# Kernel optimization log

Measured on AMD Instinct MI355X. Metric: run time of the kernel, lower is better.

The kernel has to match this reference:

```python
import jax, jax.numpy as jnp
import numpy as np


def setup_inputs() -> dict:
    key = jax.random.key(0)
    ks = jax.random.split(key, 5)
    B, S, I, H, O = 64, 2048, 128, 512, 128
    inputs = jax.random.normal(ks[0], (B, S, I), dtype=jnp.float32)
    h0 = jnp.zeros((B, H), dtype=jnp.float32)
    # Xavier-uniform for W_in / W_out, orthogonal-ish scaled for W_rec
    lim_in = float(np.sqrt(6.0 / (I + H)))
    W_in_w = jax.random.uniform(ks[1], (H, I), minval=-lim_in, maxval=lim_in, dtype=jnp.float32)
    W_in_b = jnp.zeros((H,), dtype=jnp.float32)
    # orthogonal init scaled by 0.9 (matches nn.init.orthogonal_ * 0.9)
    A = jax.random.normal(ks[2], (H, H), dtype=jnp.float32)
    Q, _ = jnp.linalg.qr(A)
    W_rec_w = (0.9 * Q).astype(jnp.float32)
    lim_out = float(np.sqrt(6.0 / (H + O)))
    W_out_w = jax.random.uniform(ks[3], (O, H), minval=-lim_out, maxval=lim_out, dtype=jnp.float32)
    W_out_b = jnp.zeros((O,), dtype=jnp.float32)
    return {
        "inputs": inputs, "h0": h0,
        "W_in_w": W_in_w, "W_in_b": W_in_b,
        "W_rec_w": W_rec_w,
        "W_out_w": W_out_w, "W_out_b": W_out_b,
    }


def reference(inputs, h0, W_in_w, W_in_b, W_rec_w, W_out_w, W_out_b):
    # Precompute the input projection for all timesteps in one big GEMM:
    # (B, S, I) @ (I, H) -> (B, S, H). Faithful: W_in(x_t) = x_t @ W_in_w.T + b.
    xin = jnp.einsum('bsi,hi->bsh', inputs, W_in_w) + W_in_b

    def step(h, x_t):  # x_t: (B, H) pre-projected input at time t
        h_new = jnp.tanh(x_t + h @ W_rec_w.T)  # W_rec has no bias
        return h_new, h_new

    # scan over time axis; move time to leading axis
    h_final, hs = jax.lax.scan(step, h0, jnp.swapaxes(xin, 0, 1))  # hs: (S, B, H)
    hs = jnp.swapaxes(hs, 0, 1)  # (B, S, H)
    outputs = jnp.einsum('bsh,oh->bso', hs, W_out_w) + W_out_b  # (B, S, O)
    return outputs, h_final
```

## Files before the change

kernel.cpp:

```cpp
#include <hip/hip_runtime.h>


typedef _Float16 half2_t __attribute__((ext_vector_type(2)));
typedef _Float16 half8_t __attribute__((ext_vector_type(8)));
typedef float    float2_t __attribute__((ext_vector_type(2)));
typedef float    float4_t __attribute__((ext_vector_type(4)));

#define BB 64
#define SS 2048
#define IN 128
#define HH 512
#define OO 128

using u32 = unsigned int;
using u64 = unsigned long long;

__device__ __forceinline__ float fdot2f(half2_t a, half2_t b, float c) {
#if __has_builtin(__builtin_amdgcn_fdot2)
    return __builtin_amdgcn_fdot2(a, b, c, false);
#else
    return c + (float)a[0] * (float)b[0] + (float)a[1] * (float)b[1];
#endif
}
__device__ __forceinline__ half2_t h2(float a, float b) {
    return half2_t{(_Float16)a, (_Float16)b};
}

__device__ __forceinline__ float fast_tanh(float x) {
    x = fminf(8.0f, fmaxf(-8.0f, x));
#if __has_builtin(__builtin_amdgcn_exp2f) && __has_builtin(__builtin_amdgcn_rcpf)
    const float t = __builtin_amdgcn_exp2f(x * 2.885390081777927f);
    return 1.0f - 2.0f * __builtin_amdgcn_rcpf(t + 1.0f);
#else
    return tanhf(x);
#endif
}

__device__ __forceinline__ void barrier_lds() {
    asm volatile("s_waitcnt lgkmcnt(0)\n\ts_barrier" ::: "memory");
}

__global__ __launch_bounds__(512, 1) void rnn_fused(
    const float* __restrict__ inputs,
    const float* __restrict__ h0,
    const float* __restrict__ W_in,
    const float* __restrict__ W_in_b,
    const float* __restrict__ W_rec,
    const float* __restrict__ W_out,
    const float* __restrict__ W_out_b,
    float* __restrict__ outp,
    float* __restrict__ hfinal,
    u64* __restrict__ hex)
{
    const int tid = threadIdx.x;
    const int bb = blockIdx.x >> 1;
    const int w  = blockIdx.x & 1;
    const int c  = tid & 7;
    const int q  = tid >> 3;
    const int og = w * 64 + q;
    const int s  = c >> 2;
    const int oc = w * 4 + (c & 3);
    const int pc = (1 - w) * 4 + (c & 3);
    const int pw = 1 - w;

    __shared__ __align__(16) half2_t hbuf[288];
    __shared__ __align__(16) half2_t xh[2][96];

    half2_t wro[4][16];
    half2_t wrp[4][16];
    half2_t wi[4][8];
    half2_t woo[16];
    half2_t wop[16];
    float bias[4];

    #pragma unroll
    for (int jj = 0; jj < 4; ++jj) {
        const int jg = w * 256 + q * 4 + jj;
        const float4_t* ro = (const float4_t*)(W_rec + jg * HH + oc * 64 + s * 32);
        const float4_t* rp = (const float4_t*)(W_rec + jg * HH + pc * 64 + s * 32);
        #pragma unroll
        for (int m = 0; m < 8; ++m) {
            const float4_t uo = ro[m];
            wro[jj][m * 2 + 0] = h2(uo[0], uo[1]);
            wro[jj][m * 2 + 1] = h2(uo[2], uo[3]);
            const float4_t up = rp[m];
            wrp[jj][m * 2 + 0] = h2(up[0], up[1]);
            wrp[jj][m * 2 + 1] = h2(up[2], up[3]);
        }
        const float4_t* irow = (const float4_t*)(W_in + jg * IN + c * 16);
        #pragma unroll
        for (int m = 0; m < 4; ++m) {
            const float4_t u = irow[m];
            wi[jj][m * 2 + 0] = h2(u[0], u[1]);
            wi[jj][m * 2 + 1] = h2(u[2], u[3]);
        }
        bias[jj] = W_in_b[jg];
    }
    {
        const float4_t* oo = (const float4_t*)(W_out + og * HH + oc * 64 + s * 32);
        const float4_t* op = (const float4_t*)(W_out + og * HH + pc * 64 + s * 32);
        #pragma unroll
        for (int m = 0; m < 8; ++m) {
            const float4_t uo = oo[m];
            woo[m * 2 + 0] = h2(uo[0], uo[1]);
            woo[m * 2 + 1] = h2(uo[2], uo[3]);
            const float4_t up = op[m];
            wop[m * 2 + 0] = h2(up[0], up[1]);
            wop[m * 2 + 1] = h2(up[2], up[3]);
        }
    }
    const float bo = W_out_b[og];

    if (tid < 256) {
        const float2_t u = *(const float2_t*)(h0 + bb * HH + tid * 2);
        const int k = tid * 2;
        hbuf[(k >> 6) * 36 + ((k & 63) >> 1)] = h2(u[0], u[1]);
    }
    if (tid >= 256 && tid < 320) {
        const int i2 = tid - 256;
        const float2_t u = *(const float2_t*)(inputs +
                              (size_t)(bb * SS + 0) * IN + i2 * 2);
        xh[0][(i2 >> 3) * 12 + (i2 & 7)] = h2(u[0], u[1]);
    }
    __syncthreads();

    for (int t = 0; t < SS; ++t) {
        const int cur = t & 1;

        float2_t xr;
        const bool xload = (tid >= 256 && tid < 320) && (t + 1 < SS);
        if (xload)
            xr = *(const float2_t*)(inputs +
                     (size_t)(bb * SS + (t + 1)) * IN + (tid - 256) * 2);

        float acc[4] = {0.f, 0.f, 0.f, 0.f};
        float oa = 0.f;
        {
            const half2_t* hb = &hbuf[oc * 36 + s * 16];
            #pragma unroll
            for (int ob = 0; ob < 4; ++ob) {
                const half8_t hv = *(const half8_t*)(hb + ob * 4);
                const half2_t p0 = __builtin_shufflevector(hv, hv, 0, 1);
                const half2_t p1 = __builtin_shufflevector(hv, hv, 2, 3);
                const half2_t p2 = __builtin_shufflevector(hv, hv, 4, 5);
                const half2_t p3 = __builtin_shufflevector(hv, hv, 6, 7);
                #pragma unroll
                for (int jj = 0; jj < 4; ++jj) {
                    acc[jj] = fdot2f(wro[jj][ob * 4 + 0], p0, acc[jj]);
                    acc[jj] = fdot2f(wro[jj][ob * 4 + 1], p1, acc[jj]);
                    acc[jj] = fdot2f(wro[jj][ob * 4 + 2], p2, acc[jj]);
                    acc[jj] = fdot2f(wro[jj][ob * 4 + 3], p3, acc[jj]);
                }
                oa = fdot2f(woo[ob * 4 + 0], p0, oa);
                oa = fdot2f(woo[ob * 4 + 1], p1, oa);
                oa = fdot2f(woo[ob * 4 + 2], p2, oa);
                oa = fdot2f(woo[ob * 4 + 3], p3, oa);
            }
        }

        const int sidx = ((bb * 2 + pw) * 2 + (cur ^ 1)) * 128 + tid;
        u64 spec = 0;
        if (t > 0 && tid < 128)
            spec = __hip_atomic_load(&hex[sidx], __ATOMIC_RELAXED,
                                     __HIP_MEMORY_SCOPE_AGENT);

        {
            const half2_t* xb = &xh[cur][c * 12];
            const half8_t xv0 = *(const half8_t*)(xb);
            const half8_t xv1 = *(const half8_t*)(xb + 4);
            const half2_t x0 = __builtin_shufflevector(xv0, xv0, 0, 1);
            const half2_t x1 = __builtin_shufflevector(xv0, xv0, 2, 3);
            const half2_t x2 = __builtin_shufflevector(xv0, xv0, 4, 5);
            const half2_t x3 = __builtin_shufflevector(xv0, xv0, 6, 7);
            const half2_t x4 = __builtin_shufflevector(xv1, xv1, 0, 1);
            const half2_t x5 = __builtin_shufflevector(xv1, xv1, 2, 3);
            const half2_t x6 = __builtin_shufflevector(xv1, xv1, 4, 5);
            const half2_t x7 = __builtin_shufflevector(xv1, xv1, 6, 7);
            #pragma unroll
            for (int jj = 0; jj < 4; ++jj) {
                acc[jj] = fdot2f(wi[jj][0], x0, acc[jj]);
                acc[jj] = fdot2f(wi[jj][1], x1, acc[jj]);
                acc[jj] = fdot2f(wi[jj][2], x2, acc[jj]);
                acc[jj] = fdot2f(wi[jj][3], x3, acc[jj]);
                acc[jj] = fdot2f(wi[jj][4], x4, acc[jj]);
                acc[jj] = fdot2f(wi[jj][5], x5, acc[jj]);
                acc[jj] = fdot2f(wi[jj][6], x6, acc[jj]);
                acc[jj] = fdot2f(wi[jj][7], x7, acc[jj]);
            }
        }

        if (t > 0 && tid < 128) {
            u64 v = spec;
            if ((u32)(v >> 32) != (u32)t) {
                do {
                    v = __hip_atomic_load(&hex[sidx], __ATOMIC_RELAXED,
                                          __HIP_MEMORY_SCOPE_AGENT);
                } while ((u32)(v >> 32) != (u32)t);
            }
            const int kg = pw * 256 + tid * 2;
            hbuf[(kg >> 6) * 36 + ((kg & 63) >> 1)] =
                __builtin_bit_cast(half2_t, (u32)v);
        }
        barrier_lds();

        {
            const half2_t* hb = &hbuf[pc * 36 + s * 16];
            #pragma unroll
            for (int ob = 0; ob < 4; ++ob) {
                const half8_t hv = *(const half8_t*)(hb + ob * 4);
                const half2_t p0 = __builtin_shufflevector(hv, hv, 0, 1);
                const half2_t p1 = __builtin_shufflevector(hv, hv, 2, 3);
                const half2_t p2 = __builtin_shufflevector(hv, hv, 4, 5);
                const half2_t p3 = __builtin_shufflevector(hv, hv, 6, 7);
                #pragma unroll
                for (int jj = 0; jj < 4; ++jj) {
                    acc[jj] = fdot2f(wrp[jj][ob * 4 + 0], p0, acc[jj]);
                    acc[jj] = fdot2f(wrp[jj][ob * 4 + 1], p1, acc[jj]);
                    acc[jj] = fdot2f(wrp[jj][ob * 4 + 2], p2, acc[jj]);
                    acc[jj] = fdot2f(wrp[jj][ob * 4 + 3], p3, acc[jj]);
                }
                oa = fdot2f(wop[ob * 4 + 0], p0, oa);
                oa = fdot2f(wop[ob * 4 + 1], p1, oa);
                oa = fdot2f(wop[ob * 4 + 2], p2, oa);
                oa = fdot2f(wop[ob * 4 + 3], p3, oa);
            }
        }

        #pragma unroll
        for (int jj = 0; jj < 4; ++jj) {
            float v = acc[jj];
            v += __shfl_xor(v, 1);
            v += __shfl_xor(v, 2);
            v += __shfl_xor(v, 4);
            acc[jj] = v;
        }
        oa += __shfl_xor(oa, 1);
        oa += __shfl_xor(oa, 2);
        oa += __shfl_xor(oa, 4);

        {
            const bool hi = (c & 1) != 0;
            const float a0 = hi ? acc[2] : acc[0];
            const float a1 = hi ? acc[3] : acc[1];
            const float b0 = hi ? bias[2] : bias[0];
            const float b1 = hi ? bias[3] : bias[1];
            const float va = fast_tanh(a0 + b0);
            const float vb = fast_tanh(a1 + b1);
            if (c < 2) {
                const half2_t hx = h2(va, vb);
                const u64 pay = (((u64)(u32)(t + 1)) << 32) |
                                (u64)__builtin_bit_cast(u32, hx);
                const int slot = ((bb * 2 + w) * 2 + cur) * 128 + q * 2 + c;
                __hip_atomic_store(&hex[slot], pay, __ATOMIC_RELAXED,
                                   __HIP_MEMORY_SCOPE_AGENT);
                const int kg = w * 256 + q * 4 + c * 2;
                hbuf[(kg >> 6) * 36 + ((kg & 63) >> 1)] = hx;
                if (t == SS - 1)
                    *(float2_t*)(&hfinal[bb * HH + w * 256 + q * 4 + c * 2]) =
                        float2_t{va, vb};
            }
            if (c == 2 && t > 0)
                outp[(size_t)(bb * SS + (t - 1)) * OO + og] = oa + bo;
        }

        if (xload) {
            const int i2 = tid - 256;
            xh[cur ^ 1][(i2 >> 3) * 12 + (i2 & 7)] = h2(xr[0], xr[1]);
        }
        barrier_lds();
    }

    if (tid < 128) {
        const int sidx = ((bb * 2 + pw) * 2 + ((SS - 1) & 1)) * 128 + tid;
        u64 v;
        do {
            v = __hip_atomic_load(&hex[sidx], __ATOMIC_RELAXED,
                                  __HIP_MEMORY_SCOPE_AGENT);
        } while ((u32)(v >> 32) != (u32)SS);
        const int kg = pw * 256 + tid * 2;
        hbuf[(kg >> 6) * 36 + ((kg & 63) >> 1)] =
            __builtin_bit_cast(half2_t, (u32)v);
    }
    __syncthreads();
    {
        float oa = 0.f;
        const half2_t* ho = &hbuf[oc * 36 + s * 16];
        const half2_t* hp = &hbuf[pc * 36 + s * 16];
        #pragma unroll
        for (int ob = 0; ob < 4; ++ob) {
            const half8_t hv = *(const half8_t*)(ho + ob * 4);
            oa = fdot2f(woo[ob * 4 + 0], __builtin_shufflevector(hv, hv, 0, 1), oa);
            oa = fdot2f(woo[ob * 4 + 1], __builtin_shufflevector(hv, hv, 2, 3), oa);
            oa = fdot2f(woo[ob * 4 + 2], __builtin_shufflevector(hv, hv, 4, 5), oa);
            oa = fdot2f(woo[ob * 4 + 3], __builtin_shufflevector(hv, hv, 6, 7), oa);
        }
        #pragma unroll
        for (int ob = 0; ob < 4; ++ob) {
            const half8_t hv = *(const half8_t*)(hp + ob * 4);
            oa = fdot2f(wop[ob * 4 + 0], __builtin_shufflevector(hv, hv, 0, 1), oa);
            oa = fdot2f(wop[ob * 4 + 1], __builtin_shufflevector(hv, hv, 2, 3), oa);
            oa = fdot2f(wop[ob * 4 + 2], __builtin_shufflevector(hv, hv, 4, 5), oa);
            oa = fdot2f(wop[ob * 4 + 3], __builtin_shufflevector(hv, hv, 6, 7), oa);
        }
        oa += __shfl_xor(oa, 1);
        oa += __shfl_xor(oa, 2);
        oa += __shfl_xor(oa, 4);
        if (c == 0)
            outp[(size_t)(bb * SS + (SS - 1)) * OO + og] = oa + bo;
    }
}

extern "C" void kernel_launch(void* const* d_in, const int* in_sizes, int n_in,
                              void* d_out, int out_size, void* d_ws, size_t ws_size,
                              hipStream_t stream) {
    const float* inputs  = (const float*)d_in[0];
    const float* h0      = (const float*)d_in[1];
    const float* W_in_w  = (const float*)d_in[2];
    const float* W_in_b  = (const float*)d_in[3];
    const float* W_rec_w = (const float*)d_in[4];
    const float* W_out_w = (const float*)d_in[5];
    const float* W_out_b = (const float*)d_in[6];

    float* out    = (float*)d_out;
    float* hfinal = out + (size_t)BB * SS * OO;
    u64* hex      = (u64*)d_ws;

    rnn_fused<<<dim3(BB * 2), dim3(512), 0, stream>>>(
        inputs, h0, W_in_w, W_in_b, W_rec_w, W_out_w, W_out_b,
        out, hfinal, hex);
}
```

Baseline: 3.730 ms.

## Add fast sc0-scoped inter-block h exchange path with handshake and fallback

Adds a second exchange buffer that paired blocks read and write using inline-asm global loads and stores with the sc0 cache bit. The aim is lower latency on the cross-block hidden-state spin-wait than agent-scope atomics give. A startup magic-value handshake checks that the partner block is co-resident and can see these writes. If the handshake fails, or a bounded spin count runs out, the code falls back to the existing atomic path. It relies on sc0 visibility semantics between CUs that may not hold, so the fallback is kept and every step writes both buffers.

```diff
diff --git a/kernel.cpp b/kernel.cpp
--- a/kernel.cpp
+++ b/kernel.cpp
@@ -11,6 +11,9 @@
 #define IN 128
 #define HH 512
 #define OO 128
+#define FAST_SPINS 16
+#define HS_SPINS 256
+#define HS_MAGIC 0x517E2026C0FFEE01ull
 
 using u32 = unsigned int;
 using u64 = unsigned long long;
@@ -38,6 +41,18 @@
 
 __device__ __forceinline__ void barrier_lds() {
     asm volatile("s_waitcnt lgkmcnt(0)\n\ts_barrier" ::: "memory");
+}
+
+__device__ __forceinline__ u64 ld_sc0(const u64* p) {
+    u64 v;
+    asm volatile("global_load_dwordx2 %0, %1, off sc0\n\t"
+                 "s_waitcnt vmcnt(0)"
+                 : "=&v"(v) : "v"(p) : "memory");
+    return v;
+}
+__device__ __forceinline__ void st_sc0(u64* p, u64 v) {
+    asm volatile("global_store_dwordx2 %0, %1, off sc0"
+                 :: "v"(p), "v"(v) : "memory");
 }
 
 __global__ __launch_bounds__(512, 1) void rnn_fused(
@@ -50,7 +65,9 @@
     const float* __restrict__ W_out_b,
     float* __restrict__ outp,
     float* __restrict__ hfinal,
-    u64* __restrict__ hex)
+    u64* __restrict__ hex,
+    u64* __restrict__ hexf,
+    int fast_ok)
 {
     const int tid = threadIdx.x;
     const int bb = blockIdx.x >> 1;
@@ -65,6 +82,10 @@
 
     __shared__ __align__(16) half2_t hbuf[288];
     __shared__ __align__(16) half2_t xh[2][96];
+    __shared__ int sfast;
+
+    if (tid == 0 && fast_ok)
+        st_sc0(&hexf[((bb * 2 + w) * 2 + 1) * 128], HS_MAGIC);
 
     half2_t wro[4][16];
     half2_t wrp[4][16];
@@ -111,6 +132,17 @@
     }
     const float bo = W_out_b[og];
 
+    if (tid == 0) {
+        int f = 0;
+        if (fast_ok) {
+            const u64* pslot = &hexf[((bb * 2 + pw) * 2 + 1) * 128];
+            for (int i = 0; i < HS_SPINS; ++i) {
+                if (ld_sc0(pslot) == HS_MAGIC) { f = 1; break; }
+            }
+        }
+        sfast = f;
+    }
+
     if (tid < 256) {
         const float2_t u = *(const float2_t*)(h0 + bb * HH + tid * 2);
         const int k = tid * 2;
@@ -123,6 +155,7 @@
         xh[0][(i2 >> 3) * 12 + (i2 & 7)] = h2(u[0], u[1]);
     }
     __syncthreads();
+    const bool fastp = sfast != 0;
 
     for (int t = 0; t < SS; ++t) {
         const int cur = t & 1;
@@ -161,8 +194,9 @@
         const int sidx = ((bb * 2 + pw) * 2 + (cur ^ 1)) * 128 + tid;
         u64 spec = 0;
         if (t > 0 && tid < 128)
-            spec = __hip_atomic_load(&hex[sidx], __ATOMIC_RELAXED,
-                                     __HIP_MEMORY_SCOPE_AGENT);
+            spec = fastp ? ld_sc0(&hexf[sidx])
+                         : __hip_atomic_load(&hex[sidx], __ATOMIC_RELAXED,
+                                             __HIP_MEMORY_SCOPE_AGENT);
 
         {
             const half2_t* xb = &xh[cur][c * 12];
@@ -191,11 +225,15 @@
 
         if (t > 0 && tid < 128) {
             u64 v = spec;
-            if ((u32)(v >> 32) != (u32)t) {
+            if (fastp && (u32)(v >> 32) != (u32)t) {
+                int sp = FAST_SPINS;
                 do {
-                    v = __hip_atomic_load(&hex[sidx], __ATOMIC_RELAXED,
-                                          __HIP_MEMORY_SCOPE_AGENT);
-                } while ((u32)(v >> 32) != (u32)t);
+                    v = ld_sc0(&hexf[sidx]);
+                } while ((u32)(v >> 32) != (u32)t && --sp > 0);
+            }
+            while ((u32)(v >> 32) != (u32)t) {
+                v = __hip_atomic_load(&hex[sidx], __ATOMIC_RELAXED,
+                                      __HIP_MEMORY_SCOPE_AGENT);
             }
             const int kg = pw * 256 + tid * 2;
             hbuf[(kg >> 6) * 36 + ((kg & 63) >> 1)] =
@@ -251,6 +289,7 @@
                 const u64 pay = (((u64)(u32)(t + 1)) << 32) |
                                 (u64)__builtin_bit_cast(u32, hx);
                 const int slot = ((bb * 2 + w) * 2 + cur) * 128 + q * 2 + c;
+                if (fastp) st_sc0(&hexf[slot], pay);
                 __hip_atomic_store(&hex[slot], pay, __ATOMIC_RELAXED,
                                    __HIP_MEMORY_SCOPE_AGENT);
                 const int kg = w * 256 + q * 4 + c * 2;
@@ -272,11 +311,17 @@
 
     if (tid < 128) {
         const int sidx = ((bb * 2 + pw) * 2 + ((SS - 1) & 1)) * 128 + tid;
-        u64 v;
-        do {
+        u64 v = 0;
+        if (fastp) {
+            int sp = FAST_SPINS;
+            do {
+                v = ld_sc0(&hexf[sidx]);
+            } while ((u32)(v >> 32) != (u32)SS && --sp > 0);
+        }
+        while ((u32)(v >> 32) != (u32)SS) {
             v = __hip_atomic_load(&hex[sidx], __ATOMIC_RELAXED,
                                   __HIP_MEMORY_SCOPE_AGENT);
-        } while ((u32)(v >> 32) != (u32)SS);
+        }
         const int kg = pw * 256 + tid * 2;
         hbuf[(kg >> 6) * 36 + ((kg & 63) >> 1)] =
             __builtin_bit_cast(half2_t, (u32)v);
@@ -323,9 +368,14 @@
 
     float* out    = (float*)d_out;
     float* hfinal = out + (size_t)BB * SS * OO;
-    u64* hex      = (u64*)d_ws;
+
+    const size_t slots = (size_t)BB * 2 * 2 * 128;
+    u64* hex  = (u64*)d_ws;
+    u64* hexf = hex + slots;
+    int fast_ok = (ws_size >= 2 * slots * sizeof(u64)) ? 1 : 0;
+    if (!fast_ok) hexf = hex;
 
     rnn_fused<<<dim3(BB * 2), dim3(512), 0, stream>>>(
         inputs, h0, W_in_w, W_in_b, W_rec_w, W_out_w, W_out_b,
-        out, hfinal, hex);
-}
+        out, hfinal, hex, hexf, fast_ok);
+}
```

Result: slower. 6.693 ms (+79.4%).

## Split RNN into input-projection, single-block recurrence, and output-projection kernels

Applied to the files above, without the earlier changes.

Replaces the fused two-block-per-batch kernel, which exchanged hidden state through global atomics, with three kernels. The first precomputes the input projection into an fp16 workspace. The second runs the recurrence with one block per batch, keeping 6 of every 8 W_rec rows in registers and the other 2 in LDS, and overwrites the workspace with the hidden states. The third computes the output projection from those stored states. This removes the cross-block spin-wait handshake per timestep and takes the output GEMM off the serial path. In exchange it adds large workspace traffic, and each recurrence block does twice the per-step work, running only 64 blocks. The old fused kernel is kept as a fallback when the workspace is too small.

```diff
diff --git a/kernel.cpp b/kernel.cpp
--- a/kernel.cpp
+++ b/kernel.cpp
@@ -12,6 +12,7 @@
 #define HH 512
 #define OO 128
 
+using u16 = unsigned short;
 using u32 = unsigned int;
 using u64 = unsigned long long;
 
@@ -25,7 +26,6 @@
 __device__ __forceinline__ half2_t h2(float a, float b) {
     return half2_t{(_Float16)a, (_Float16)b};
 }
-
 __device__ __forceinline__ float fast_tanh(float x) {
     x = fminf(8.0f, fmaxf(-8.0f, x));
 #if __has_builtin(__builtin_amdgcn_exp2f) && __has_builtin(__builtin_amdgcn_rcpf)
@@ -35,22 +35,234 @@
     return tanhf(x);
 #endif
 }
-
 __device__ __forceinline__ void barrier_lds() {
     asm volatile("s_waitcnt lgkmcnt(0)\n\ts_barrier" ::: "memory");
 }
 
-__global__ __launch_bounds__(512, 1) void rnn_fused(
+__device__ __forceinline__ float red8(float v) {
+    int i;
+    i = __builtin_amdgcn_update_dpp(0, __builtin_bit_cast(int, v),
+                                    0xB1, 0xF, 0xF, true);
+    v += __builtin_bit_cast(float, i);
+    i = __builtin_amdgcn_update_dpp(0, __builtin_bit_cast(int, v),
+                                    0x4E, 0xF, 0xF, true);
+    v += __builtin_bit_cast(float, i);
+    i = __builtin_amdgcn_update_dpp(0, __builtin_bit_cast(int, v),
+                                    0x141, 0xF, 0xF, true);
+    v += __builtin_bit_cast(float, i);
+    return v;
+}
+__device__ __forceinline__ float sel8(const float a[8], int c) {
+    float v = a[0];
+    v = (c == 1) ? a[1] : v;  v = (c == 2) ? a[2] : v;
+    v = (c == 3) ? a[3] : v;  v = (c == 4) ? a[4] : v;
+    v = (c == 5) ? a[5] : v;  v = (c == 6) ? a[6] : v;
+    v = (c == 7) ? a[7] : v;
+    return v;
+}
+
+__global__ __launch_bounds__(512, 2) void rnn_xin(
     const float* __restrict__ inputs,
-    const float* __restrict__ h0,
     const float* __restrict__ W_in,
     const float* __restrict__ W_in_b,
+    u16* __restrict__ xws)
+{
+    const int tid = threadIdx.x;
+    const int c   = tid & 7;
+    const int q   = tid >> 3;
+    const float bmy = W_in_b[tid];
+
+    half2_t wi8[8][8];
+    #pragma unroll
+    for (int jj = 0; jj < 8; ++jj) {
+        const float4_t* r = (const float4_t*)(W_in + (q * 8 + jj) * IN + c * 16);
+        #pragma unroll
+        for (int m = 0; m < 4; ++m) {
+            const float4_t u = r[m];
+            wi8[jj][m * 2 + 0] = h2(u[0], u[1]);
+            wi8[jj][m * 2 + 1] = h2(u[2], u[3]);
+        }
+    }
+
+    const int row0 = blockIdx.x * 512;
+    for (int r = 0; r < 512; ++r) {
+        const size_t row = row0 + r;
+        const float4_t* xr = (const float4_t*)(inputs + row * IN + c * 16);
+        half2_t xv[8];
+        #pragma unroll
+        for (int m = 0; m < 4; ++m) {
+            const float4_t u = xr[m];
+            xv[m * 2 + 0] = h2(u[0], u[1]);
+            xv[m * 2 + 1] = h2(u[2], u[3]);
+        }
+        float acc[8] = {0, 0, 0, 0, 0, 0, 0, 0};
+        #pragma unroll
+        for (int jj = 0; jj < 8; ++jj)
+            #pragma unroll
+            for (int m = 0; m < 8; ++m)
+                acc[jj] = fdot2f(wi8[jj][m], xv[m], acc[jj]);
+        #pragma unroll
+        for (int jj = 0; jj < 8; ++jj) acc[jj] = red8(acc[jj]);
+        const float out = sel8(acc, c) + bmy;
+        const _Float16 hf = (_Float16)out;
+        xws[row * HH + tid] = __builtin_bit_cast(u16, hf);
+    }
+}
+
+#define REC_STEP(RB, WB, T)                                                  \
+    do {                                                                     \
+        u16 xn = 0;                                                          \
+        if ((T) + 1 < SS) xn = xp[(size_t)((T) + 1) * HH + tid];             \
+        float acc[8] = {0, 0, 0, 0, 0, 0, 0, 0};                             \
+        const half2_t* hb = &(RB)[c * 36];                                   \
+        _Pragma("unroll")                                                    \
+        for (int kb = 0; kb < 8; ++kb) {                                     \
+            const half8_t hv = *(const half8_t*)(hb + kb * 4);               \
+            const half2_t p0 = __builtin_shufflevector(hv, hv, 0, 1);        \
+            const half2_t p1 = __builtin_shufflevector(hv, hv, 2, 3);        \
+            const half2_t p2 = __builtin_shufflevector(hv, hv, 4, 5);        \
+            const half2_t p3 = __builtin_shufflevector(hv, hv, 6, 7);        \
+            _Pragma("unroll")                                                \
+            for (int jj = 0; jj < 6; ++jj) {                                 \
+                acc[jj] = fdot2f(wr[jj][kb * 4 + 0], p0, acc[jj]);           \
+                acc[jj] = fdot2f(wr[jj][kb * 4 + 1], p1, acc[jj]);           \
+                acc[jj] = fdot2f(wr[jj][kb * 4 + 2], p2, acc[jj]);           \
+                acc[jj] = fdot2f(wr[jj][kb * 4 + 3], p3, acc[jj]);           \
+            }                                                                \
+            const half8_t w6 = *(const half8_t*)(wb6 + (size_t)kb * 2048);   \
+            acc[6] = fdot2f(__builtin_shufflevector(w6, w6, 0, 1), p0, acc[6]); \
+            acc[6] = fdot2f(__builtin_shufflevector(w6, w6, 2, 3), p1, acc[6]); \
+            acc[6] = fdot2f(__builtin_shufflevector(w6, w6, 4, 5), p2, acc[6]); \
+            acc[6] = fdot2f(__builtin_shufflevector(w6, w6, 6, 7), p3, acc[6]); \
+            const half8_t w7 = *(const half8_t*)(wb7 + (size_t)kb * 2048);   \
+            acc[7] = fdot2f(__builtin_shufflevector(w7, w7, 0, 1), p0, acc[7]); \
+            acc[7] = fdot2f(__builtin_shufflevector(w7, w7, 2, 3), p1, acc[7]); \
+            acc[7] = fdot2f(__builtin_shufflevector(w7, w7, 4, 5), p2, acc[7]); \
+            acc[7] = fdot2f(__builtin_shufflevector(w7, w7, 6, 7), p3, acc[7]); \
+        }                                                                    \
+        _Pragma("unroll")                                                    \
+        for (int jj = 0; jj < 8; ++jj) acc[jj] = red8(acc[jj]);              \
+        const float hv_new = fast_tanh(sel8(acc, c) + (float)xr);            \
+        const _Float16 hf = (_Float16)hv_new;                                \
+        xp[(size_t)(T) * HH + tid] = __builtin_bit_cast(u16, hf);            \
+        ((_Float16*)(WB))[(tid >> 6) * 72 + (tid & 63)] = hf;                \
+        if ((T) == SS - 1) hfinal[bb * HH + tid] = hv_new;                   \
+        xr = __builtin_bit_cast(_Float16, xn);                               \
+        barrier_lds();                                                       \
+    } while (0)
+
+__global__ __launch_bounds__(512, 2) void rnn_rec(
+    const float* __restrict__ h0,
     const float* __restrict__ W_rec,
+    u16* __restrict__ xws,
+    float* __restrict__ hfinal)
+{
+    const int tid = threadIdx.x;
+    const int bb  = blockIdx.x;
+    const int c   = tid & 7;
+    const int q   = tid >> 3;
+
+    __shared__ __align__(16) half2_t wlin[2 * 8 * 512 * 4];
+    __shared__ __align__(16) half2_t hbuf[2][288];
+
+    half2_t wr[6][32];
+    #pragma unroll
+    for (int jj = 0; jj < 6; ++jj) {
+        const float4_t* r = (const float4_t*)(W_rec + (q * 8 + jj) * HH + c * 64);
+        #pragma unroll
+        for (int m = 0; m < 16; ++m) {
+            const float4_t u = r[m];
+            wr[jj][m * 2 + 0] = h2(u[0], u[1]);
+            wr[jj][m * 2 + 1] = h2(u[2], u[3]);
+        }
+    }
+    #pragma unroll
+    for (int jl = 0; jl < 2; ++jl) {
+        const int j = q * 8 + 6 + jl;
+        #pragma unroll
+        for (int kb = 0; kb < 8; ++kb) {
+            const float4_t u0 = *(const float4_t*)(W_rec + j * HH + c * 64 + kb * 8);
+            const float4_t u1 = *(const float4_t*)(W_rec + j * HH + c * 64 + kb * 8 + 4);
+            half8_t pack = half8_t{
+                (_Float16)u0[0], (_Float16)u0[1], (_Float16)u0[2], (_Float16)u0[3],
+                (_Float16)u1[0], (_Float16)u1[1], (_Float16)u1[2], (_Float16)u1[3]};
+            *(half8_t*)&wlin[((jl * 8 + kb) * 512 + tid) * 4] = pack;
+        }
+    }
+    ((_Float16*)hbuf[0])[(tid >> 6) * 72 + (tid & 63)] = (_Float16)h0[bb * HH + tid];
+
+    u16* xp = xws + (size_t)bb * SS * HH;
+    _Float16 xr = __builtin_bit_cast(_Float16, xp[tid]);
+    __syncthreads();
+
+    const half2_t* wb6 = &wlin[(size_t)tid * 4];
+    const half2_t* wb7 = &wlin[(size_t)(8 * 512 + tid) * 4];
+
+    for (int t = 0; t < SS; t += 2) {
+        REC_STEP(hbuf[0], hbuf[1], t);
+        REC_STEP(hbuf[1], hbuf[0], t + 1);
+    }
+}
+
+__global__ __launch_bounds__(512, 2) void rnn_out(
+    const u16* __restrict__ xws,
     const float* __restrict__ W_out,
     const float* __restrict__ W_out_b,
-    float* __restrict__ outp,
-    float* __restrict__ hfinal,
-    u64* __restrict__ hex)
+    float* __restrict__ outp)
+{
+    const int tid = threadIdx.x;
+    const int c   = tid & 7;
+    const int wv  = tid >> 6;
+    const int lq  = (tid >> 3) & 7;
+    const int o0  = wv * 16 + lq * 2;
+
+    half2_t wo2[2][32];
+    #pragma unroll
+    for (int oo = 0; oo < 2; ++oo) {
+        const float4_t* r = (const float4_t*)(W_out + (o0 + oo) * HH + c * 64);
+        #pragma unroll
+        for (int m = 0; m < 16; ++m) {
+            const float4_t u = r[m];
+            wo2[oo][m * 2 + 0] = h2(u[0], u[1]);
+            wo2[oo][m * 2 + 1] = h2(u[2], u[3]);
+        }
+    }
+    const float b0 = W_out_b[o0], b1 = W_out_b[o0 + 1];
+
+    const int row0 = blockIdx.x * 512;
+    for (int r = 0; r < 512; ++r) {
+        const size_t row = row0 + r;
+        const _Float16* hsrow = (const _Float16*)xws + row * HH + c * 64;
+        float a0 = 0.f, a1 = 0.f;
+        #pragma unroll
+        for (int kb = 0; kb < 8; ++kb) {
+            const half8_t hv = *(const half8_t*)(hsrow + kb * 8);
+            const half2_t p0 = __builtin_shufflevector(hv, hv, 0, 1);
+            const half2_t p1 = __builtin_shufflevector(hv, hv, 2, 3);
+            const half2_t p2 = __builtin_shufflevector(hv, hv, 4, 5);
+            const half2_t p3 = __builtin_shufflevector(hv, hv, 6, 7);
+            a0 = fdot2f(wo2[0][kb * 4 + 0], p0, a0);
+            a0 = fdot2f(wo2[0][kb * 4 + 1], p1, a0);
+            a0 = fdot2f(wo2[0][kb * 4 + 2], p2, a0);
+            a0 = fdot2f(wo2[0][kb * 4 + 3], p3, a0);
+            a1 = fdot2f(wo2[1][kb * 4 + 0], p0, a1);
+            a1 = fdot2f(wo2[1][kb * 4 + 1], p1, a1);
+            a1 = fdot2f(wo2[1][kb * 4 + 2], p2, a1);
+            a1 = fdot2f(wo2[1][kb * 4 + 3], p3, a1);
+        }
+        a0 = red8(a0);
+        a1 = red8(a1);
+        if (c == 0)
+            *(float2_t*)(outp + row * OO + o0) = float2_t{a0 + b0, a1 + b1};
+    }
+}
+
+__global__ __launch_bounds__(512, 1) void rnn_fused_fb(
+    const float* __restrict__ inputs, const float* __restrict__ h0,
+    const float* __restrict__ W_in, const float* __restrict__ W_in_b,
+    const float* __restrict__ W_rec, const float* __restrict__ W_out,
+    const float* __restrict__ W_out_b, float* __restrict__ outp,
+    float* __restrict__ hfinal, u64* __restrict__ hex)
 {
     const int tid = threadIdx.x;
     const int bb = blockIdx.x >> 1;
@@ -66,12 +278,8 @@
     __shared__ __align__(16) half2_t hbuf[288];
     __shared__ __align__(16) half2_t xh[2][96];
 
-    half2_t wro[4][16];
-    half2_t wrp[4][16];
-    half2_t wi[4][8];
-    half2_t woo[16];
-    half2_t wop[16];
-    float bias[4];
+    half2_t wro[4][16]; half2_t wrp[4][16]; half2_t wi[4][8];
+    half2_t woo[16]; half2_t wop[16]; float bias[4];
 
     #pragma unroll
     for (int jj = 0; jj < 4; ++jj) {
@@ -118,20 +326,17 @@
     }
     if (tid >= 256 && tid < 320) {
         const int i2 = tid - 256;
-        const float2_t u = *(const float2_t*)(inputs +
-                              (size_t)(bb * SS + 0) * IN + i2 * 2);
+        const float2_t u = *(const float2_t*)(inputs + (size_t)(bb * SS) * IN + i2 * 2);
         xh[0][(i2 >> 3) * 12 + (i2 & 7)] = h2(u[0], u[1]);
     }
     __syncthreads();
 
     for (int t = 0; t < SS; ++t) {
         const int cur = t & 1;
-
         float2_t xr;
         const bool xload = (tid >= 256 && tid < 320) && (t + 1 < SS);
         if (xload)
-            xr = *(const float2_t*)(inputs +
-                     (size_t)(bb * SS + (t + 1)) * IN + (tid - 256) * 2);
+            xr = *(const float2_t*)(inputs + (size_t)(bb * SS + (t + 1)) * IN + (tid - 256) * 2);
 
         float acc[4] = {0.f, 0.f, 0.f, 0.f};
         float oa = 0.f;
@@ -157,13 +362,11 @@
                 oa = fdot2f(woo[ob * 4 + 3], p3, oa);
             }
         }
-
         const int sidx = ((bb * 2 + pw) * 2 + (cur ^ 1)) * 128 + tid;
         u64 spec = 0;
         if (t > 0 && tid < 128)
             spec = __hip_atomic_load(&hex[sidx], __ATOMIC_RELAXED,
                                      __HIP_MEMORY_SCOPE_AGENT);
-
         {
             const half2_t* xb = &xh[cur][c * 12];
             const half8_t xv0 = *(const half8_t*)(xb);
@@ -188,7 +391,6 @@
                 acc[jj] = fdot2f(wi[jj][7], x7, acc[jj]);
             }
         }
-
         if (t > 0 && tid < 128) {
             u64 v = spec;
             if ((u32)(v >> 32) != (u32)t) {
@@ -202,7 +404,6 @@
                 __builtin_bit_cast(half2_t, (u32)v);
         }
         barrier_lds();
-
         {
             const half2_t* hb = &hbuf[pc * 36 + s * 16];
             #pragma unroll
@@ -225,7 +426,6 @@
                 oa = fdot2f(wop[ob * 4 + 3], p3, oa);
             }
         }
-
         #pragma unroll
         for (int jj = 0; jj < 4; ++jj) {
             float v = acc[jj];
@@ -237,7 +437,6 @@
         oa += __shfl_xor(oa, 1);
         oa += __shfl_xor(oa, 2);
         oa += __shfl_xor(oa, 4);
-
         {
             const bool hi = (c & 1) != 0;
             const float a0 = hi ? acc[2] : acc[0];
@@ -262,7 +461,6 @@
             if (c == 2 && t > 0)
                 outp[(size_t)(bb * SS + (t - 1)) * OO + og] = oa + bo;
         }
-
         if (xload) {
             const int i2 = tid - 256;
             xh[cur ^ 1][(i2 >> 3) * 12 + (i2 & 7)] = h2(xr[0], xr[1]);
@@ -323,9 +521,17 @@
 
     float* out    = (float*)d_out;
     float* hfinal = out + (size_t)BB * SS * OO;
-    u64* hex      = (u64*)d_ws;
-
-    rnn_fused<<<dim3(BB * 2), dim3(512), 0, stream>>>(
-        inputs, h0, W_in_w, W_in_b, W_rec_w, W_out_w, W_out_b,
-        out, hfinal, hex);
-}
+
+    const size_t xin_bytes = (size_t)BB * SS * HH * sizeof(u16);
+    if (ws_size >= xin_bytes) {
+        u16* xws = (u16*)d_ws;
+        rnn_xin<<<dim3(256), dim3(512), 0, stream>>>(inputs, W_in_w, W_in_b, xws);
+        rnn_rec<<<dim3(BB), dim3(512), 0, stream>>>(h0, W_rec_w, xws, hfinal);
+        rnn_out<<<dim3(256), dim3(512), 0, stream>>>(xws, W_out_w, W_out_b, out);
+    } else {
+        u64* hex = (u64*)d_ws;
+        rnn_fused_fb<<<dim3(BB * 2), dim3(512), 0, stream>>>(
+            inputs, h0, W_in_w, W_in_b, W_rec_w, W_out_w, W_out_b,
+            out, hfinal, hex);
+    }
+}
```

Result: slower. 4.462 ms (+19.6%).
